# Kernel optimization log

Measured on AMD Instinct MI355X. Metric: run time of the kernel, lower is better.

Reference implementation:

```python
import jax, jax.numpy as jnp
from jax import lax
import numpy as np

B = 1024          # batch
N = 30            # max_nodes
IN_DIM = 32       # latent dim
NT, ET = 5, 3     # node / edge type counts
CH = [64, 32, 32, 1]
KS = [(3, 7), (3, 3), (3, 3), (3, 5)]
ST = [(1, 1), (1, 4), (1, 2), (1, 2)]
PD = [(0, 0), (0, 0), (1, 0), (1, 4)]   # torch-style ConvTranspose2d padding
BN_EPS = 1e-5
SMALL = 1e-7


def setup_inputs() -> dict:
    key = jax.random.key(0)
    ks = jax.random.split(key, 5)
    inp = {"Z": jax.random.normal(ks[0], (B, IN_DIM), jnp.float32)}
    cin = [1] + CH[:-1]
    for i in range(4):
        fan_in = KS[i][0] * KS[i][1] * cin[i]
        w = jax.random.normal(ks[i + 1], (KS[i][0], KS[i][1], cin[i], CH[i]), jnp.float32)
        inp[f"W{i+1}"] = w * np.float32(1.0 / np.sqrt(fan_in))
    for i in range(3):
        inp[f"g{i+1}"] = jnp.ones((CH[i],), jnp.float32)
        inp[f"b{i+1}"] = jnp.zeros((CH[i],), jnp.float32)
    return inp


def _deconv(x, w, s, k, p):
    # torch ConvTranspose2d(padding=p) == conv with lhs_dilation=s and pad k-1-p per side
    pads = ((k[0] - 1 - p[0],) * 2, (k[1] - 1 - p[1],) * 2)
    return lax.conv_transpose(x, w, s, pads, dimension_numbers=("NHWC", "HWIO", "NHWC"))


def _bn_relu(x, g, b):
    m = x.mean((0, 1, 2))
    v = x.var((0, 1, 2))
    return jax.nn.relu(g * (x - m) * lax.rsqrt(v + BN_EPS) + b)


def _generator(Z, Ws, gbs):
    x = Z.reshape(B, IN_DIM, 1, 1)                      # NHWC: (B, 32, 1, 1)
    for i in range(4):
        x = _deconv(x, Ws[i], ST[i], KS[i], PD[i])
        if i < 3:
            x = _bn_relu(x, *gbs[i])
    return x.reshape(B, N, -1)                          # (B, 30, 126)


def reference(Z, W1, W2, W3, W4, g1, b1, g2, b2, g3, b3):
    out = _generator(Z, (W1, W2, W3, W4), ((g1, b1), (g2, b2), (g3, b3)))
    X = jax.nn.softmax(out[:, :, : NT + 1], axis=-1)    # (B, N, 6) soft node types
    iu = jnp.triu_indices(N, 1)                         # 435 upper-triangular edges
    oe = out[:, :, NT + 1:].reshape(B, N, N, ET + 1)[:, iu[0], iu[1], :]
    ve = jax.nn.softmax(oe, axis=-1)                    # (B, 435, 4) soft edge types
    all_edges = jnp.stack(iu).astype(jnp.int32)         # (2, 435)
    edge_index = jnp.concatenate([all_edges, all_edges[::-1]], axis=-1)  # (2, 870)
    batch = jnp.repeat(jnp.arange(B), N)
    edge_attr = jnp.concatenate([ve, ve], axis=1)       # (B, 870, 4)
    # vectorized hard selection: one fused argmax->one-hot pass instead of O(B*N) python loops
    X_hard = jax.nn.one_hot(jnp.argmax(X, axis=-1), NT + 1, dtype=X.dtype)
    ve_hard = jax.nn.one_hot(jnp.argmax(ve, axis=-1), ET + 1, dtype=ve.dtype)
    ea_hard = jnp.concatenate([ve_hard, ve_hard], axis=1)
    log_prob = (jnp.sum(jnp.log(X + SMALL) * X_hard)
                + jnp.sum(jnp.log(ve + SMALL) * ve_hard))
    return (X[:, :, 1:], edge_index, edge_attr[:, :, 1:],
            1.0 - X[:, :, 0], 1.0 - edge_attr[:, :, 0], batch,
            X_hard[:, :, 1:], ea_hard[:, :, 1:],
            1.0 - X_hard[:, :, 0], 1.0 - ea_hard[:, :, 0], log_prob)
```

## Files before the change

kernel.cpp:

```cpp
#include <hip/hip_runtime.h>
#include <hip/hip_bf16.h>

typedef __hip_bfloat16 bf16;
typedef __attribute__((ext_vector_type(8))) short short8;
typedef __attribute__((ext_vector_type(4))) float floatx4;
typedef __bf16 bf16x8 __attribute__((ext_vector_type(8)));

#define OFF_A1 0
#define OFF_C1 64
#define OFF_A2 128
#define OFF_C2 160
#define OFF_A3 192
#define OFF_C3 224
#define OFF_LP 256
#define OFF_P1S 512
#define OFF_P1Q 66048
#define OFF_P2S 131584
#define OFF_P2Q 205312

#define FW2_BYTE 2295808u
#define FW3_BYTE 2332672u
#define FW4_BYTE 2351104u
#define X2_BYTE  33546240u
#define X3_BYTE  97247232u
#define O4_BYTE  227008512u

#define P3S_ABS 56752128
#define P3Q_ABS 56973312

#define OUT0 0
#define OUT1 153600
#define OUT2 155340
#define OUT3 2827980
#define OUT4 2858700
#define OUT5 3749580
#define OUT6 3780300
#define OUT7 3933900
#define OUT8 6606540
#define OUT9 6637260
#define OUT10 7528140

__device__ __forceinline__ bf16 f2b(float v){ return __float2bfloat16(v); }
__device__ __forceinline__ unsigned short f2bu(float v){ bf16 h = __float2bfloat16(v); return *(unsigned short*)&h; }

__device__ __forceinline__ floatx4 mfma16(short8 a, short8 b, floatx4 c){
  return __builtin_amdgcn_mfma_f32_16x16x32_bf16(__builtin_bit_cast(bf16x8, a),
                                                 __builtin_bit_cast(bf16x8, b), c, 0, 0, 0);
}

__device__ __forceinline__ unsigned int nrm2(unsigned int u, float a0, float c0, float a1, float c1){
  float x0 = __uint_as_float(u << 16);
  float x1 = __uint_as_float(u & 0xffff0000u);
  float y0 = fmaxf(fmaf(a0, x0, c0), 0.f);
  float y1 = fmaxf(fmaf(a1, x1, c1), 0.f);
  return (unsigned int)f2bu(y0) | ((unsigned int)f2bu(y1) << 16);
}

__device__ __forceinline__ void gload_lds16(const unsigned short* g, unsigned short* lds){
  __builtin_amdgcn_global_load_lds((const __attribute__((address_space(1))) unsigned int*)g,
                                   (__attribute__((address_space(3))) unsigned int*)lds, 16, 0, 0);
}

__global__ __launch_bounds__(256) void k_prep(const float* __restrict__ W2, const float* __restrict__ W3,
                                              const float* __restrict__ W4,
                                              unsigned short* __restrict__ fw2, unsigned short* __restrict__ fw3,
                                              unsigned short* __restrict__ fw4){
  const int t = blockIdx.x*256 + threadIdx.x;
  if (t < 2304){
    const int L = t & 63, kc = (t>>6)&1, mt = (t>>7)&1, tap = t>>8;
    const int co = mt*16 + (L&15), ci0 = kc*32 + ((L>>4)&3)*8;
    #pragma unroll
    for (int j = 0; j < 8; ++j)
      fw2[(size_t)t*8 + j] = f2bu(W2[((size_t)tap*64 + ci0 + j)*32 + co]);
  }
  if (t < 1152){
    const int L = t & 63, mt = (t>>6)&1, tap = t>>7;
    const int co = mt*16 + (L&15), ci0 = ((L>>4)&3)*8;
    #pragma unroll
    for (int j = 0; j < 8; ++j)
      fw3[(size_t)t*8 + j] = f2bu(W3[((size_t)tap*32 + ci0 + j)*32 + co]);
  }
  if (t < 1920){
    const int L = t & 63, d = (t>>6) % 10, r = t / 640;
    const int m = L & 15, ci0 = ((L>>4)&3)*8;
    const int kw = 2*d - m;
    #pragma unroll
    for (int j = 0; j < 8; ++j)
      fw4[(size_t)t*8 + j] = (kw >= 0 && kw < 5) ? f2bu(W4[(r*5 + kw)*32 + ci0 + j])
                                                 : (unsigned short)0;
  }
}

__global__ __launch_bounds__(256) void k_dc1(const float* __restrict__ Z, const float* __restrict__ W1,
                                             float* __restrict__ ws){
  const int b = blockIdx.x, t = threadIdx.x;
  __shared__ float zs[32];
  __shared__ float w1s[3*7*64];
  __shared__ float red[256];
  if (t < 32) zs[t] = Z[b*32 + t];
  for (int i = t; i < 1344; i += 256) w1s[i] = W1[i];
  __syncthreads();
  float lsum = 0.f, lsq = 0.f;
  for (int idx = t; idx < 15232; idx += 256){
    int co = idx & 63;
    int wo = (idx >> 6) % 7;
    int ho = idx / 448;
    int kw = 6 - wo;
    float y = 0.f;
    #pragma unroll
    for (int kh = 0; kh < 3; ++kh){
      int hi = ho + kh - 2;
      if (hi >= 0 && hi < 32) y += zs[hi] * w1s[(kh*7 + kw)*64 + co];
    }
    lsum += y; lsq += y*y;
  }
  red[t] = lsum; __syncthreads();
  if (t < 64) ws[OFF_P1S + b*64 + t] = red[t] + red[t+64] + red[t+128] + red[t+192];
  __syncthreads();
  red[t] = lsq; __syncthreads();
  if (t < 64) ws[OFF_P1Q + b*64 + t] = red[t] + red[t+64] + red[t+128] + red[t+192];
}

__global__ __launch_bounds__(256) void k_fin(float* __restrict__ ws, const float* __restrict__ g,
                                             const float* __restrict__ bb, int ps, int pq, int npart,
                                             int nch, float inv_n, int ao, int co, int zlp){
  const int c = blockIdx.x, t = threadIdx.x;
  __shared__ float r1[256], r2[256];
  float s = 0.f, q = 0.f;
  for (int i = t; i < npart; i += 256){ s += ws[ps + i*nch + c]; q += ws[pq + i*nch + c]; }
  r1[t] = s; r2[t] = q; __syncthreads();
  for (int off = 128; off > 0; off >>= 1){
    if (t < off){ r1[t] += r1[t+off]; r2[t] += r2[t+off]; }
    __syncthreads();
  }
  if (t == 0){
    float m  = r1[0] * inv_n;
    float v  = r2[0] * inv_n - m*m;
    float is = rsqrtf(v + 1e-5f);
    float a  = g[c] * is;
    ws[ao + c] = a;
    ws[co + c] = bb[c] - a*m;
  }
  if (zlp && c == 0 && t == 0) ws[OFF_LP] = 0.f;
}

__global__ __launch_bounds__(256) void k2(const float* __restrict__ Z, const float* __restrict__ W1,
                                          const unsigned short* __restrict__ fw2,
                                          unsigned short* __restrict__ x2, float* __restrict__ ws){
  const int t = threadIdx.x;
  const int b0 = blockIdx.x*16, ho = blockIdx.y;
  __shared__ unsigned short sa[21*1024];
  __shared__ float zs[16][32];
  __shared__ float w1s[1344];
  __shared__ float sa1[64], sc1[64];
  __shared__ float sred[2][4][32];
  if (t < 64){ sa1[t] = ws[OFF_A1+t]; sc1[t] = ws[OFF_C1+t]; }
  for (int i = t; i < 512; i += 256) zs[i>>5][i&31] = Z[(b0 + (i>>5))*32 + (i&31)];
  for (int i = t; i < 1344; i += 256) w1s[i] = W1[i];
  __syncthreads();
  for (int c = t; c < 21*128; c += 256){
    const int p = c >> 7, g = c & 127;
    const int r = p/7, wi = p - r*7;
    const int hi = ho - 2 + r;
    const int b = g >> 3, kc = (g >> 2) & 1, j = g & 3;
    const int ci0 = kc*32 + j*8;
    unsigned int pk[4] = {0,0,0,0};
    if (hi >= 0 && hi < 34){
      const float* wp = &w1s[(6 - wi)*64 + ci0];
      #pragma unroll
      for (int e = 0; e < 8; e += 2){
        float y0 = 0.f, y1 = 0.f;
        #pragma unroll
        for (int kh = 0; kh < 3; ++kh){
          const int q = hi + kh - 2;
          if (q >= 0 && q < 32){
            float zv = zs[b][q];
            y0 += zv * wp[kh*448 + e];
            y1 += zv * wp[kh*448 + e + 1];
          }
        }
        float u0 = fmaxf(fmaf(sa1[ci0+e],   y0, sc1[ci0+e]),   0.f);
        float u1 = fmaxf(fmaf(sa1[ci0+e+1], y1, sc1[ci0+e+1]), 0.f);
        pk[e>>1] = (unsigned int)f2bu(u0) | ((unsigned int)f2bu(u1) << 16);
      }
    }
    *(uint4*)(sa + (size_t)p*1024 + kc*512 + (j*16 + b)*8) = *(uint4*)pk;
  }
  __syncthreads();
  const int w = t>>6, L = t&63;
  floatx4 acc[8][2];
  #pragma unroll
  for (int i = 0; i < 8; ++i){ acc[i][0] = (floatx4)0.f; acc[i][1] = (floatx4)0.f; }
  const int wiA = 2*w, wiB = (w < 3) ? 2*w + 1 : 2*w;
  for (int r = 0; r < 3; ++r){
    short8 af[3][2][2];
    #pragma unroll
    for (int kw = 0; kw < 3; ++kw)
      #pragma unroll
      for (int mt = 0; mt < 2; ++mt)
        #pragma unroll
        for (int kc = 0; kc < 2; ++kc)
          af[kw][mt][kc] = *(const short8*)(fw2 + ((((size_t)(r*3+kw)*2 + mt)*2 + kc)*64 + L)*8);
    const short8* pA = (const short8*)(sa + (size_t)(r*7 + wiA)*1024);
    const short8* pB = (const short8*)(sa + (size_t)(r*7 + wiB)*1024);
    short8 fa0 = pA[L], fa1 = pA[64+L];
    short8 fb0 = pB[L], fb1 = pB[64+L];
    #pragma unroll
    for (int idx = 0; idx < 8; ++idx){
      if (idx == 3 || idx == 7) continue;
      const int kw = (2 - idx) & 3;
      const int half = idx >> 2;
      if (half && w == 3) continue;
      short8 f0 = half ? fb0 : fa0;
      short8 f1 = half ? fb1 : fa1;
      #pragma unroll
      for (int mt = 0; mt < 2; ++mt){
        acc[idx][mt] = mfma16(af[kw][mt][0], f0, acc[idx][mt]);
        acc[idx][mt] = mfma16(af[kw][mt][1], f1, acc[idx][mt]);
      }
    }
  }
  const int bL = L & 15, jj = (L>>4)&3;
  float ss[2][4] = {{0,0,0,0},{0,0,0,0}}, sq[2][4] = {{0,0,0,0},{0,0,0,0}};
  #pragma unroll
  for (int idx = 0; idx < 8; ++idx){
    if (8*w + idx >= 27) continue;
    #pragma unroll
    for (int mt = 0; mt < 2; ++mt){
      floatx4 a = acc[idx][mt];
      ss[mt][0] += a.x; ss[mt][1] += a.y; ss[mt][2] += a.z; ss[mt][3] += a.w;
      sq[mt][0] += a.x*a.x; sq[mt][1] += a.y*a.y; sq[mt][2] += a.z*a.z; sq[mt][3] += a.w*a.w;
    }
  }
  #pragma unroll
  for (int mt = 0; mt < 2; ++mt)
    #pragma unroll
    for (int r2 = 0; r2 < 4; ++r2){
      float v1 = ss[mt][r2], v2 = sq[mt][r2];
      for (int d = 1; d < 16; d <<= 1){ v1 += __shfl_xor(v1, d, 64); v2 += __shfl_xor(v2, d, 64); }
      if (bL == 0){
        int cch = mt*16 + jj*4 + r2;
        sred[0][w][cch] = v1;
        sred[1][w][cch] = v2;
      }
    }
  __syncthreads();
  if (t < 64){
    const int cch = t & 31, j2 = t >> 5;
    float tot = sred[j2][0][cch] + sred[j2][1][cch] + sred[j2][2][cch] + sred[j2][3][cch];
    const int bid = blockIdx.y*64 + blockIdx.x;
    ws[(j2 ? OFF_P2Q : OFF_P2S) + bid*32 + cch] = tot;
  }
  unsigned short* st = sa + w*4608;
  #pragma unroll
  for (int idx = 0; idx < 8; ++idx){
    if (8*w + idx >= 27) continue;
    #pragma unroll
    for (int mt = 0; mt < 2; ++mt){
      floatx4 a = acc[idx][mt];
      uint2 pk;
      pk.x = (unsigned int)f2bu(a.x) | ((unsigned int)f2bu(a.y) << 16);
      pk.y = (unsigned int)f2bu(a.z) | ((unsigned int)f2bu(a.w) << 16);
      *(uint2*)(st + idx*576 + bL*36 + mt*16 + jj*4) = pk;
    }
  }
  const int sb = L >> 2, q2 = L & 3;
  #pragma unroll
  for (int idx = 0; idx < 8; ++idx){
    const int wo = 8*w + idx;
    if (wo >= 27) continue;
    uint4 v = *(const uint4*)(st + idx*576 + sb*36 + q2*8);
    *(uint4*)(x2 + ((size_t)(ho*27+wo)*1024 + b0 + sb)*32 + q2*8) = v;
  }
}

__global__ __launch_bounds__(256) void k3(const unsigned short* __restrict__ x2, const unsigned short* __restrict__ fw3,
                                          unsigned short* __restrict__ x3, float* __restrict__ ws){
  const int t = threadIdx.x;
  const int b0 = blockIdx.x*16, hop = blockIdx.y, z = blockIdx.z;
  const int ho0 = hop*2;
  const int wib = (z == 0) ? 0 : ((z == 1) ? 8 : 17);
  __shared__ unsigned short sa[44*512];
  __shared__ float sa2[32], sc2[32];
  __shared__ float sred[2][4][32];
  if (t < 32){ sa2[t] = ws[OFF_A2+t]; sc2[t] = ws[OFF_C2+t]; }
  const int w = t>>6, L = t&63;
  const int bL = L & 15, jL = (L>>4)&3, ci0 = jL*8;
  for (int p = w; p < 44; p += 4){
    const int row = p/11, wl = p - row*11;
    const int hi = ho0 - 1 + row, wi = wib + wl;
    unsigned short* dst = sa + p*512;
    if (hi >= 0 && hi < 36 && wi < 27){
      const unsigned short* src = x2 + ((size_t)(hi*27 + wi)*1024 + b0 + bL)*32 + ci0;
      gload_lds16(src, dst);
    } else {
      *(uint4*)(dst + L*8) = make_uint4(0,0,0,0);
    }
  }
  __syncthreads();
  {
    float an[8], cn[8];
    #pragma unroll
    for (int e = 0; e < 8; ++e){ an[e] = sa2[ci0+e]; cn[e] = sc2[ci0+e]; }
    for (int i = t; i < 44*64; i += 256){
      const int p = i >> 6;
      const int row = p/11, wl = p - row*11;
      const int hi = ho0 - 1 + row, wi = wib + wl;
      if (hi >= 0 && hi < 36 && wi < 27){
        uint4 v = *(uint4*)(sa + (size_t)i*8);
        v.x = nrm2(v.x, an[0], cn[0], an[1], cn[1]);
        v.y = nrm2(v.y, an[2], cn[2], an[3], cn[3]);
        v.z = nrm2(v.z, an[4], cn[4], an[5], cn[5]);
        v.w = nrm2(v.w, an[6], cn[6], an[7], cn[7]);
        *(uint4*)(sa + (size_t)i*8) = v;
      }
    }
  }
  __syncthreads();
  const int s0 = z*18 + ((w==0) ? 0 : (w==1) ? 6 : (w==2) ? 10 : 14);
  const int h2 = s0 >> 1;
  const int nvalid = (w==0) ? 6 : ((z==2 && w==3) ? 5 : 4);
  floatx4 acc[2][6][2];
  #pragma unroll
  for (int hoL = 0; hoL < 2; ++hoL)
    #pragma unroll
    for (int i = 0; i < 6; ++i){ acc[hoL][i][0] = (floatx4)0.f; acc[hoL][i][1] = (floatx4)0.f; }
  for (int r = 0; r < 3; ++r){
    short8 af[3][2];
    #pragma unroll
    for (int kw = 0; kw < 3; ++kw)
      #pragma unroll
      for (int mt = 0; mt < 2; ++mt)
        af[kw][mt] = *(const short8*)(fw3 + (((size_t)(r*3+kw)*2 + mt)*64 + L)*8);
    #pragma unroll
    for (int hoL = 0; hoL < 2; ++hoL){
      const int row = hoL + r;
      short8 bb[4];
      #pragma unroll
      for (int d = 0; d < 4; ++d){
        const int wl = h2 - 1 + d - wib;
        short8 v = (short8)0;
        if (wl >= 0 && wl <= 10)
          v = *(const short8*)(sa + (size_t)(row*11 + wl)*512 + L*8);
        bb[d] = v;
      }
      #pragma unroll
      for (int idx = 0; idx < 6; ++idx){
        if (idx >= nvalid) continue;
        if ((idx & 1) == 0){
          const int d = idx >> 1;
          #pragma unroll
          for (int mt = 0; mt < 2; ++mt){
            acc[hoL][idx][mt] = mfma16(af[0][mt], bb[d],   acc[hoL][idx][mt]);
            acc[hoL][idx][mt] = mfma16(af[2][mt], bb[d+1], acc[hoL][idx][mt]);
          }
        } else {
          const int d = ((idx - 1) >> 1) + 1;
          #pragma unroll
          for (int mt = 0; mt < 2; ++mt)
            acc[hoL][idx][mt] = mfma16(af[1][mt], bb[d], acc[hoL][idx][mt]);
        }
      }
    }
  }
  const int jj = jL;
  float ss[2][4] = {{0,0,0,0},{0,0,0,0}}, sq[2][4] = {{0,0,0,0},{0,0,0,0}};
  #pragma unroll
  for (int hoL = 0; hoL < 2; ++hoL)
    #pragma unroll
    for (int idx = 0; idx < 6; ++idx){
      if (idx >= nvalid) continue;
      #pragma unroll
      for (int mt = 0; mt < 2; ++mt){
        floatx4 a = acc[hoL][idx][mt];
        ss[mt][0] += a.x; ss[mt][1] += a.y; ss[mt][2] += a.z; ss[mt][3] += a.w;
        sq[mt][0] += a.x*a.x; sq[mt][1] += a.y*a.y; sq[mt][2] += a.z*a.z; sq[mt][3] += a.w*a.w;
      }
    }
  #pragma unroll
  for (int mt = 0; mt < 2; ++mt)
    #pragma unroll
    for (int r2 = 0; r2 < 4; ++r2){
      float v1 = ss[mt][r2], v2 = sq[mt][r2];
      for (int d = 1; d < 16; d <<= 1){ v1 += __shfl_xor(v1, d, 64); v2 += __shfl_xor(v2, d, 64); }
      if (bL == 0){
        int cch = mt*16 + jj*4 + r2;
        sred[0][w][cch] = v1;
        sred[1][w][cch] = v2;
      }
    }
  __syncthreads();
  if (t < 64){
    const int cch = t & 31, j2 = t >> 5;
    float tot = sred[j2][0][cch] + sred[j2][1][cch] + sred[j2][2][cch] + sred[j2][3][cch];
    const int bid = (z*18 + hop)*64 + blockIdx.x;
    ws[(j2 ? P3Q_ABS : P3S_ABS) + bid*32 + cch] = tot;
  }
  unsigned short* st = sa + w*3456;
  const int sb = L >> 2, q2 = L & 3;
  #pragma unroll
  for (int hoL = 0; hoL < 2; ++hoL){
    #pragma unroll
    for (int idx = 0; idx < 6; ++idx){
      if (idx >= nvalid) continue;
      #pragma unroll
      for (int mt = 0; mt < 2; ++mt){
        floatx4 a = acc[hoL][idx][mt];
        uint2 pk;
        pk.x = (unsigned int)f2bu(a.x) | ((unsigned int)f2bu(a.y) << 16);
        pk.y = (unsigned int)f2bu(a.z) | ((unsigned int)f2bu(a.w) << 16);
        *(uint2*)(st + idx*576 + bL*36 + mt*16 + jj*4) = pk;
      }
    }
    #pragma unroll
    for (int idx = 0; idx < 6; ++idx){
      if (idx >= nvalid) continue;
      const int wo = s0 + idx;
      uint4 v = *(const uint4*)(st + idx*576 + sb*36 + q2*8);
      *(uint4*)(x3 + ((size_t)((ho0+hoL)*55+wo)*1024 + b0 + sb)*32 + q2*8) = v;
    }
  }
}

__global__ __launch_bounds__(256) void k_dc4(const unsigned short* __restrict__ x3,
                                             const unsigned short* __restrict__ fw4,
                                             float* __restrict__ o4, const float* __restrict__ ws){
  const int t = threadIdx.x;
  const int w = t >> 6, L = t & 63;
  const int b0 = blockIdx.x*16;
  const int ho0 = blockIdx.y*3;
  __shared__ float a3s[32], c3s[32];
  __shared__ unsigned short fa4[30*512];
  __shared__ float rowbuf[16*113];
  if (t < 32){ a3s[t] = ws[OFF_A3+t]; c3s[t] = ws[OFF_C3+t]; }
  for (int i = t; i < 1920; i += 256)
    *(uint4*)(fa4 + (size_t)i*8) = *(const uint4*)(fw4 + (size_t)i*8);
  __syncthreads();
  const int bL = L & 15, jj = (L>>4)&3, ci0 = jj*8;
  float an[8], cn[8];
  #pragma unroll
  for (int e = 0; e < 8; ++e){ an[e] = a3s[ci0+e]; cn[e] = c3s[ci0+e]; }
  floatx4 acc[2][3];
  #pragma unroll
  for (int i = 0; i < 2; ++i)
    #pragma unroll
    for (int h = 0; h < 3; ++h) acc[i][h] = (floatx4)0.f;
  for (int e = 0; e < 5; ++e){
    const int hi = ho0 - 1 + e;
    if (hi < 0 || hi >= 36) continue;
    #pragma unroll
    for (int ts = 0; ts < 2; ++ts){
      const int T = w + ts*4;
      if (T >= 7) continue;
      #pragma unroll 5
      for (int d = 0; d < 10; ++d){
        const int wi = 8*T + d;
        short8 bf;
        if (wi < 55){
          uint4 v = *(const uint4*)(x3 + ((size_t)(hi*55 + wi)*1024 + b0 + bL)*32 + ci0);
          v.x = nrm2(v.x, an[0], cn[0], an[1], cn[1]);
          v.y = nrm2(v.y, an[2], cn[2], an[3], cn[3]);
          v.z = nrm2(v.z, an[4], cn[4], an[5], cn[5]);
          v.w = nrm2(v.w, an[6], cn[6], an[7], cn[7]);
          bf = __builtin_bit_cast(short8, v);
        } else {
          bf = (short8)0;
        }
        #pragma unroll
        for (int hl = 0; hl < 3; ++hl){
          const int r = e - hl;
          if (r < 0 || r > 2) continue;
          short8 af = *(const short8*)(fa4 + ((size_t)(r*10 + d)*64 + L)*8);
          acc[ts][hl] = mfma16(af, bf, acc[ts][hl]);
        }
      }
    }
  }
  #pragma unroll
  for (int hl = 0; hl < 3; ++hl){
    __syncthreads();
    #pragma unroll
    for (int ts = 0; ts < 2; ++ts){
      const int T = w + ts*4;
      if (T >= 7) continue;
      floatx4 a = acc[ts][hl];
      float vals[4] = {a.x, a.y, a.z, a.w};
      #pragma unroll
      for (int reg = 0; reg < 4; ++reg){
        const int wo = 16*T + jj*4 + reg;
        if (wo < 105) rowbuf[bL*113 + wo] = vals[reg];
      }
    }
    __syncthreads();
    const int ho = ho0 + hl;
    for (int i = t; i < 1680; i += 256){
      const int bb = i / 105, wo = i - bb*105;
      o4[(size_t)(b0 + bb)*3780 + ho*105 + wo] = rowbuf[bb*113 + wo];
    }
  }
}

__global__ __launch_bounds__(256) void k_node(const float* __restrict__ o4, float* __restrict__ dout,
                                              float* __restrict__ ws){
  const int t = threadIdx.x;
  const int tg = blockIdx.x*256 + t;
  __shared__ float red[256];
  float lp = 0.f;
  {
    int b = tg / 30, n = tg - b*30;
    const float* p = o4 + (size_t)b*3780 + n*126;
    float l[6]; float mx = -1e30f;
    #pragma unroll
    for (int j = 0; j < 6; ++j){ l[j] = p[j]; mx = fmaxf(mx, l[j]); }
    float e[6]; float s = 0.f;
    #pragma unroll
    for (int j = 0; j < 6; ++j){ e[j] = expf(l[j] - mx); s += e[j]; }
    float inv = 1.f / s;
    int am = 0; float best = e[0];
    #pragma unroll
    for (int j = 1; j < 6; ++j){ if (e[j] > best){ best = e[j]; am = j; } }
    #pragma unroll
    for (int j = 0; j < 5; ++j) dout[OUT0 + (size_t)tg*5 + j] = e[j+1]*inv;
    dout[OUT3 + tg] = 1.f - e[0]*inv;
    #pragma unroll
    for (int j = 0; j < 5; ++j) dout[OUT6 + (size_t)tg*5 + j] = (am == j+1) ? 1.f : 0.f;
    dout[OUT8 + tg] = (am != 0) ? 1.f : 0.f;
    dout[OUT5 + tg] = (float)b;
    lp = logf(best*inv + 1e-7f);
  }
  red[t] = lp; __syncthreads();
  for (int off = 128; off > 0; off >>= 1){ if (t < off) red[t] += red[t+off]; __syncthreads(); }
  if (t == 0) atomicAdd(&ws[OFF_LP], red[0]);
}

__global__ __launch_bounds__(256) void k_edge(const float* __restrict__ o4, float* __restrict__ dout,
                                              float* __restrict__ ws){
  const int t = threadIdx.x;
  const int tg = blockIdx.x*256 + t;
  __shared__ float red[256];
  float lp = 0.f;
  {
    int b = tg / 435, k = tg - b*435;
    int i = (int)((59.0f - sqrtf((float)(3481 - 8*k))) * 0.5f);
    int rem = k - ((i*(59 - i)) >> 1);
    if (rem < 0){ i -= 1; rem = k - ((i*(59 - i)) >> 1); }
    else if (rem >= 29 - i){ rem -= 29 - i; i += 1; }
    int j = i + 1 + rem;
    const float* p = o4 + (size_t)b*3780 + i*126 + 6 + j*4;
    float l0 = p[0], l1 = p[1], l2 = p[2], l3 = p[3];
    float mx = fmaxf(fmaxf(l0, l1), fmaxf(l2, l3));
    float e0 = expf(l0-mx), e1 = expf(l1-mx), e2 = expf(l2-mx), e3 = expf(l3-mx);
    float inv = 1.f / (e0 + e1 + e2 + e3);
    float pr0 = e0*inv, pr1 = e1*inv, pr2 = e2*inv, pr3 = e3*inv;
    int am = 0; float best = pr0;
    if (pr1 > best){ best = pr1; am = 1; }
    if (pr2 > best){ best = pr2; am = 2; }
    if (pr3 > best){ best = pr3; am = 3; }
    size_t e1i = (size_t)b*870 + k, e2i = e1i + 435;
    dout[OUT2 + e1i*3 + 0] = pr1; dout[OUT2 + e1i*3 + 1] = pr2; dout[OUT2 + e1i*3 + 2] = pr3;
    dout[OUT2 + e2i*3 + 0] = pr1; dout[OUT2 + e2i*3 + 1] = pr2; dout[OUT2 + e2i*3 + 2] = pr3;
    dout[OUT4 + e1i] = 1.f - pr0;  dout[OUT4 + e2i] = 1.f - pr0;
    float h1 = (am == 1) ? 1.f : 0.f, h2 = (am == 2) ? 1.f : 0.f, h3 = (am == 3) ? 1.f : 0.f;
    dout[OUT7 + e1i*3 + 0] = h1; dout[OUT7 + e1i*3 + 1] = h2; dout[OUT7 + e1i*3 + 2] = h3;
    dout[OUT7 + e2i*3 + 0] = h1; dout[OUT7 + e2i*3 + 1] = h2; dout[OUT7 + e2i*3 + 2] = h3;
    dout[OUT9 + e1i] = (am != 0) ? 1.f : 0.f;  dout[OUT9 + e2i] = (am != 0) ? 1.f : 0.f;
    if (b == 0){
      dout[OUT1 + k]        = (float)i;
      dout[OUT1 + 435 + k]  = (float)j;
      dout[OUT1 + 870 + k]  = (float)j;
      dout[OUT1 + 1305 + k] = (float)i;
    }
    lp = logf(best + 1e-7f);
  }
  red[t] = lp; __syncthreads();
  for (int off = 128; off > 0; off >>= 1){ if (t < off) red[t] += red[t+off]; __syncthreads(); }
  if (t == 0) atomicAdd(&ws[OFF_LP], red[0]);
}

__global__ void k_lp_copy(float* __restrict__ dout, const float* __restrict__ ws){
  if (threadIdx.x == 0 && blockIdx.x == 0) dout[OUT10] = ws[OFF_LP];
}

extern "C" void kernel_launch(void* const* d_in, const int* in_sizes, int n_in,
                              void* d_out, int out_size, void* d_ws, size_t ws_size,
                              hipStream_t stream) {
  const float* Z  = (const float*)d_in[0];
  const float* W1 = (const float*)d_in[1];
  const float* W2 = (const float*)d_in[2];
  const float* W3 = (const float*)d_in[3];
  const float* W4 = (const float*)d_in[4];
  const float* g1 = (const float*)d_in[5];
  const float* b1 = (const float*)d_in[6];
  const float* g2 = (const float*)d_in[7];
  const float* b2 = (const float*)d_in[8];
  const float* g3 = (const float*)d_in[9];
  const float* b3 = (const float*)d_in[10];

  float* ws  = (float*)d_ws;
  char*  wsb = (char*)d_ws;
  unsigned short* fw2 = (unsigned short*)(wsb + FW2_BYTE);
  unsigned short* fw3 = (unsigned short*)(wsb + FW3_BYTE);
  unsigned short* fw4 = (unsigned short*)(wsb + FW4_BYTE);
  unsigned short* x2u = (unsigned short*)(wsb + X2_BYTE);
  unsigned short* x3u = (unsigned short*)(wsb + X3_BYTE);
  float*          o4  = (float*)(wsb + O4_BYTE);
  float* dout = (float*)d_out;
  (void)in_sizes; (void)n_in; (void)out_size; (void)ws_size;

  k_prep<<<dim3(9), dim3(256), 0, stream>>>(W2, W3, W4, fw2, fw3, fw4);
  k_dc1<<<dim3(1024), dim3(256), 0, stream>>>(Z, W1, ws);
  k_fin<<<dim3(64), dim3(256), 0, stream>>>(ws, g1, b1, OFF_P1S, OFF_P1Q, 1024, 64,
                                            1.f/243712.f, OFF_A1, OFF_C1, 0);
  k2<<<dim3(64, 36), dim3(256), 0, stream>>>(Z, W1, fw2, x2u, ws);
  k_fin<<<dim3(32), dim3(256), 0, stream>>>(ws, g2, b2, OFF_P2S, OFF_P2Q, 2304, 32,
                                            1.f/995328.f, OFF_A2, OFF_C2, 0);
  k3<<<dim3(64, 18, 3), dim3(256), 0, stream>>>(x2u, fw3, x3u, ws);
  k_fin<<<dim3(32), dim3(256), 0, stream>>>(ws, g3, b3, P3S_ABS, P3Q_ABS, 3456, 32,
                                            1.f/2027520.f, OFF_A3, OFF_C3, 1);
  k_dc4<<<dim3(64, 12), dim3(256), 0, stream>>>(x3u, fw4, o4, ws);
  k_node<<<dim3(120), dim3(256), 0, stream>>>(o4, dout, ws);
  k_edge<<<dim3(1740), dim3(256), 0, stream>>>(o4, dout, ws);
  k_lp_copy<<<dim3(1), dim3(64), 0, stream>>>(dout, ws);
}
```

Baseline: 349.8 us.

## Precompute normalized layer-1 activations once and stream them into k2 via LDS loads

Adds a k1n kernel that computes the BN+ReLU'd first deconv output once per (row, column, batch group) in bf16, already in the swizzled layout k2 uses. k2 then fills shared memory with direct global-to-LDS copies instead of recomputing layer 1 from Z and W1. Before, each output row recomputed three input rows, so this removes about 3x redundant arithmetic. The cost is an extra launch and a global write plus read of the intermediate, which reuses the X3 buffer region before k3 writes to it.

```diff
diff --git a/kernel.cpp b/kernel.cpp
--- a/kernel.cpp
+++ b/kernel.cpp
@@ -25,6 +25,8 @@
 #define X3_BYTE  97247232u
 #define O4_BYTE  227008512u
 
+#define A1N_BYTE X3_BYTE
+
 #define P3S_ABS 56752128
 #define P3Q_ABS 56973312
 
@@ -144,50 +146,65 @@
   if (zlp && c == 0 && t == 0) ws[OFF_LP] = 0.f;
 }
 
-__global__ __launch_bounds__(256) void k2(const float* __restrict__ Z, const float* __restrict__ W1,
+__global__ __launch_bounds__(256) void k1n(const float* __restrict__ Z, const float* __restrict__ W1,
+                                           const float* __restrict__ ws, unsigned short* __restrict__ a1n){
+  const int bg = blockIdx.x, hi = blockIdx.y, t = threadIdx.x;
+  __shared__ float zr[16][4];
+  __shared__ float w1s[1344];
+  __shared__ float a1s[64], c1s[64];
+  if (t < 64){ a1s[t] = ws[OFF_A1+t]; c1s[t] = ws[OFF_C1+t]; }
+  if (t < 64){
+    const int b = t >> 2, kh = t & 3;
+    float v = 0.f;
+    if (kh < 3){
+      const int q = hi + kh - 2;
+      if (q >= 0 && q < 32) v = Z[(bg*16 + b)*32 + q];
+    }
+    zr[b][kh] = v;
+  }
+  for (int i = t; i < 1344; i += 256) w1s[i] = W1[i];
+  __syncthreads();
+  for (int c = t; c < 896; c += 256){
+    const int wi = c >> 7, g = c & 127;
+    const int kc = g >> 6, j = (g >> 4) & 3, b = g & 15;
+    const int ci0 = kc*32 + j*8;
+    const float* wp = &w1s[(6 - wi)*64 + ci0];
+    const float z0 = zr[b][0], z1 = zr[b][1], z2 = zr[b][2];
+    unsigned int pk[4];
+    #pragma unroll
+    for (int e = 0; e < 8; e += 2){
+      float y0 = z0*wp[e]       + z1*wp[448+e]   + z2*wp[896+e];
+      float y1 = z0*wp[e+1]     + z1*wp[448+e+1] + z2*wp[896+e+1];
+      float u0 = fmaxf(fmaf(a1s[ci0+e],   y0, c1s[ci0+e]),   0.f);
+      float u1 = fmaxf(fmaf(a1s[ci0+e+1], y1, c1s[ci0+e+1]), 0.f);
+      pk[e>>1] = (unsigned int)f2bu(u0) | ((unsigned int)f2bu(u1) << 16);
+    }
+    *(uint4*)(a1n + ((size_t)(hi*7 + wi)*64 + bg)*1024 + g*8) = *(uint4*)pk;
+  }
+}
+
+__global__ __launch_bounds__(256) void k2(const unsigned short* __restrict__ a1n,
                                           const unsigned short* __restrict__ fw2,
                                           unsigned short* __restrict__ x2, float* __restrict__ ws){
   const int t = threadIdx.x;
-  const int b0 = blockIdx.x*16, ho = blockIdx.y;
+  const int bx = blockIdx.x, b0 = bx*16, ho = blockIdx.y;
   __shared__ unsigned short sa[21*1024];
-  __shared__ float zs[16][32];
-  __shared__ float w1s[1344];
-  __shared__ float sa1[64], sc1[64];
   __shared__ float sred[2][4][32];
-  if (t < 64){ sa1[t] = ws[OFF_A1+t]; sc1[t] = ws[OFF_C1+t]; }
-  for (int i = t; i < 512; i += 256) zs[i>>5][i&31] = Z[(b0 + (i>>5))*32 + (i&31)];
-  for (int i = t; i < 1344; i += 256) w1s[i] = W1[i];
-  __syncthreads();
-  for (int c = t; c < 21*128; c += 256){
-    const int p = c >> 7, g = c & 127;
+  const int w = t>>6, L = t&63;
+  for (int p = w; p < 21; p += 4){
     const int r = p/7, wi = p - r*7;
     const int hi = ho - 2 + r;
-    const int b = g >> 3, kc = (g >> 2) & 1, j = g & 3;
-    const int ci0 = kc*32 + j*8;
-    unsigned int pk[4] = {0,0,0,0};
+    unsigned short* dst = sa + p*1024;
     if (hi >= 0 && hi < 34){
-      const float* wp = &w1s[(6 - wi)*64 + ci0];
-      #pragma unroll
-      for (int e = 0; e < 8; e += 2){
-        float y0 = 0.f, y1 = 0.f;
-        #pragma unroll
-        for (int kh = 0; kh < 3; ++kh){
-          const int q = hi + kh - 2;
-          if (q >= 0 && q < 32){
-            float zv = zs[b][q];
-            y0 += zv * wp[kh*448 + e];
-            y1 += zv * wp[kh*448 + e + 1];
-          }
-        }
-        float u0 = fmaxf(fmaf(sa1[ci0+e],   y0, sc1[ci0+e]),   0.f);
-        float u1 = fmaxf(fmaf(sa1[ci0+e+1], y1, sc1[ci0+e+1]), 0.f);
-        pk[e>>1] = (unsigned int)f2bu(u0) | ((unsigned int)f2bu(u1) << 16);
-      }
-    }
-    *(uint4*)(sa + (size_t)p*1024 + kc*512 + (j*16 + b)*8) = *(uint4*)pk;
-  }
-  __syncthreads();
-  const int w = t>>6, L = t&63;
+      const unsigned short* src = a1n + ((size_t)(hi*7 + wi)*64 + bx)*1024;
+      gload_lds16(src + L*8,       dst);
+      gload_lds16(src + 512 + L*8, dst + 512);
+    } else {
+      *(uint4*)(dst + L*8) = make_uint4(0,0,0,0);
+      *(uint4*)(dst + 512 + L*8) = make_uint4(0,0,0,0);
+    }
+  }
+  __syncthreads();
   floatx4 acc[8][2];
   #pragma unroll
   for (int i = 0; i < 8; ++i){ acc[i][0] = (floatx4)0.f; acc[i][1] = (floatx4)0.f; }
@@ -601,6 +618,7 @@
   unsigned short* fw2 = (unsigned short*)(wsb + FW2_BYTE);
   unsigned short* fw3 = (unsigned short*)(wsb + FW3_BYTE);
   unsigned short* fw4 = (unsigned short*)(wsb + FW4_BYTE);
+  unsigned short* a1n = (unsigned short*)(wsb + A1N_BYTE);
   unsigned short* x2u = (unsigned short*)(wsb + X2_BYTE);
   unsigned short* x3u = (unsigned short*)(wsb + X3_BYTE);
   float*          o4  = (float*)(wsb + O4_BYTE);
@@ -611,7 +629,8 @@
   k_dc1<<<dim3(1024), dim3(256), 0, stream>>>(Z, W1, ws);
   k_fin<<<dim3(64), dim3(256), 0, stream>>>(ws, g1, b1, OFF_P1S, OFF_P1Q, 1024, 64,
                                             1.f/243712.f, OFF_A1, OFF_C1, 0);
-  k2<<<dim3(64, 36), dim3(256), 0, stream>>>(Z, W1, fw2, x2u, ws);
+  k1n<<<dim3(64, 34), dim3(256), 0, stream>>>(Z, W1, ws, a1n);
+  k2<<<dim3(64, 36), dim3(256), 0, stream>>>(a1n, fw2, x2u, ws);
   k_fin<<<dim3(32), dim3(256), 0, stream>>>(ws, g2, b2, OFF_P2S, OFF_P2Q, 2304, 32,
                                             1.f/995328.f, OFF_A2, OFF_C2, 0);
   k3<<<dim3(64, 18, 3), dim3(256), 0, stream>>>(x2u, fw3, x3u, ws);
```

Result: faster. 331.8 us (-5.1%).
